# Performance work log

Measured on AMD Instinct MI355X. Metric: run time of the kernel, lower is better.

Reference implementation:

```python
import jax, jax.numpy as jnp
import numpy as np

B, T, C, H = 2, 2048, 1024, 16
D = C // H  # head dim = 64

def setup_inputs() -> dict:
    key = jax.random.key(0)
    k1, k2, k3 = jax.random.split(key, 3)
    x = jax.random.normal(k1, (B, T, C), dtype=jnp.float32)
    Wqkv = jax.random.normal(k2, (C, 3 * C), dtype=jnp.float32) * (1.0 / np.sqrt(C))
    bqkv = jnp.zeros((3 * C,), dtype=jnp.float32)
    Wo = jax.random.normal(k3, (C, C), dtype=jnp.float32) * (1.0 / np.sqrt(C))
    bo = jnp.zeros((C,), dtype=jnp.float32)
    return {"x": x, "Wqkv": Wqkv, "bqkv": bqkv, "Wo": Wo, "bo": bo}

def reference(x, Wqkv, bqkv, Wo, bo):
    b, t, c = x.shape
    qkv = x @ Wqkv + bqkv                              # [B,T,3C]
    q, k, v = jnp.split(qkv, 3, axis=-1)
    # [B,T,C] -> [B,H,T,D]
    q = q.reshape(b, t, H, D).transpose(0, 2, 1, 3)
    k = k.reshape(b, t, H, D).transpose(0, 2, 1, 3)
    v = v.reshape(b, t, H, D).transpose(0, 2, 1, 3)
    scores = jnp.einsum('bhqd,bhkd->bhqk', q, k) * (1.0 / np.sqrt(D))
    causal = jnp.tril(jnp.ones((t, t), dtype=bool))
    scores = jnp.where(causal, scores, -jnp.inf)
    probs = jax.nn.softmax(scores, axis=-1)           # dropout p=0 -> identity
    out = jnp.einsum('bhqk,bhkd->bhqd', probs, v)
    out = out.transpose(0, 2, 1, 3).reshape(b, t, c)
    return out @ Wo + bo
```

## Files before the change

### kernel.cpp

```cpp
#include <hip/hip_runtime.h>
#include <hip/hip_bf16.h>

typedef __attribute__((ext_vector_type(8))) short bf16x8;
typedef __attribute__((ext_vector_type(4))) short bf16x4;
typedef __attribute__((ext_vector_type(4))) float f32x4;

static __device__ __forceinline__ __hip_bfloat16 f2b(float f) {
    return __float2bfloat16(f);
}
static __device__ __forceinline__ unsigned pack2(float a, float b) {
    unsigned ua = (unsigned)__bfloat16_as_ushort(__float2bfloat16(a));
    unsigned ub = (unsigned)__bfloat16_as_ushort(__float2bfloat16(b));
    return ua | (ub << 16);
}
static __device__ __forceinline__ float exp2fast(float x) {
    return __builtin_amdgcn_exp2f(x);
}

#define QSCALE 0.1803368801111f

__global__ __launch_bounds__(256) void k_prep(
    const float* __restrict__ x, __hip_bfloat16* __restrict__ xb,
    const float* __restrict__ Wqkv, __hip_bfloat16* __restrict__ WqkvT,
    const float* __restrict__ Wo, __hip_bfloat16* __restrict__ WoT)
{
    const int bx = blockIdx.x;
    if (bx < 2048) {
        int i = bx * 256 + threadIdx.x;
        const int stride = 2048 * 256;
        for (; i < 1048576; i += stride) {
            float4 v = reinterpret_cast<const float4*>(x)[i];
            __hip_bfloat16* o = xb + 4 * (size_t)i;
            o[0] = f2b(v.x); o[1] = f2b(v.y); o[2] = f2b(v.z); o[3] = f2b(v.w);
        }
        return;
    }
    __shared__ float tile[32][33];
    const float* in;
    __hip_bfloat16* outp;
    int R, Cn, c0, r0;
    if (bx < 5120) {
        const int b = bx - 2048;
        in = Wqkv; outp = WqkvT; R = 1024; Cn = 3072;
        c0 = (b % 96) * 32; r0 = (b / 96) * 32;
    } else {
        const int b = bx - 5120;
        in = Wo; outp = WoT; R = 1024; Cn = 1024;
        c0 = (b & 31) * 32; r0 = (b >> 5) * 32;
    }
    const int tx = threadIdx.x & 31, ty = threadIdx.x >> 5;
#pragma unroll
    for (int i = 0; i < 32; i += 8)
        tile[ty + i][tx] = in[(size_t)(r0 + ty + i) * Cn + c0 + tx];
    __syncthreads();
#pragma unroll
    for (int i = 0; i < 32; i += 8)
        outp[(size_t)(c0 + ty + i) * R + r0 + tx] = f2b(tile[tx][ty + i]);
}

#define QK_STAGE(buf, kt)                                                       \
    {                                                                           \
        const int k0_ = (kt) << 5;                                              \
        _Pragma("unroll")                                                       \
        for (int i = 0; i < 2; ++i) {                                           \
            const int idx = i * 256 + tid;                                      \
            const int r_ = idx >> 2;                                            \
            const int j_ = idx & 3;                                             \
            const int js_ = j_ ^ ((r_ >> 1) & 3);                               \
            __builtin_amdgcn_global_load_lds(                                   \
                (const __attribute__((address_space(1))) void*)(A + (size_t)(m0 + r_) * K + k0_ + js_ * 8), \
                (__attribute__((address_space(3))) void*)(&As[buf][r_][j_ * 8]), 16, 0, 0); \
        }                                                                       \
        _Pragma("unroll")                                                       \
        for (int i = 0; i < 2; ++i) {                                           \
            const int idx = i * 256 + tid;                                      \
            const int r_ = idx >> 2;                                            \
            const int j_ = idx & 3;                                             \
            const int js_ = j_ ^ ((r_ >> 1) & 3);                               \
            __builtin_amdgcn_global_load_lds(                                   \
                (const __attribute__((address_space(1))) void*)(Bt + (size_t)(n0 + r_) * K + k0_ + js_ * 8), \
                (__attribute__((address_space(3))) void*)(&Bs[buf][r_][j_ * 8]), 16, 0, 0); \
        }                                                                       \
    }

__global__ __launch_bounds__(256, 3) void k_gemm_qkv(
    const __hip_bfloat16* __restrict__ A,
    const __hip_bfloat16* __restrict__ Bt,
    const float* __restrict__ bias,
    int K,
    __hip_bfloat16* __restrict__ Qb,
    __hip_bfloat16* __restrict__ Kb,
    __hip_bfloat16* __restrict__ Vt)
{
    __shared__ __hip_bfloat16 As[3][128][32];
    __shared__ __hip_bfloat16 Bs[3][128][32];

    const int tid = threadIdx.x;
    const int lane = tid & 63;
    const int wid = tid >> 6;
    const int wm = wid >> 1, wn = wid & 1;
    const int m0 = blockIdx.y * 128, n0 = blockIdx.x * 128;
    const int l15 = lane & 15, lg = lane >> 4;
    const int rchunk = (lg ^ ((l15 >> 1) & 3)) * 8;

    f32x4 acc[4][4] = {};
    const int nt = K >> 5;

    QK_STAGE(0, 0);
    QK_STAGE(1, 1);
    asm volatile("s_waitcnt vmcnt(4)" ::: "memory");
    __builtin_amdgcn_sched_barrier(0);
    __builtin_amdgcn_s_barrier();
    __builtin_amdgcn_sched_barrier(0);

    for (int t = 0; t < nt; ++t) {
        const int cur = t % 3;
        if (t + 2 < nt) {
            const int nxt = (t + 2) % 3;
            QK_STAGE(nxt, t + 2);
        }
        bf16x8 a[4], bb[4];
#pragma unroll
        for (int m = 0; m < 4; ++m)
            a[m] = *(const bf16x8*)&As[cur][wm * 64 + m * 16 + l15][rchunk];
#pragma unroll
        for (int n = 0; n < 4; ++n)
            bb[n] = *(const bf16x8*)&Bs[cur][wn * 64 + n * 16 + l15][rchunk];
        __builtin_amdgcn_s_setprio(1);
#pragma unroll
        for (int m = 0; m < 4; ++m)
#pragma unroll
            for (int n = 0; n < 4; ++n)
                acc[m][n] = __builtin_amdgcn_mfma_f32_16x16x32_bf16(a[m], bb[n], acc[m][n], 0, 0, 0);
        __builtin_amdgcn_s_setprio(0);
        __builtin_amdgcn_sched_barrier(0);
        if (t + 2 < nt)
            asm volatile("s_waitcnt vmcnt(4)" ::: "memory");
        else
            asm volatile("s_waitcnt vmcnt(0)" ::: "memory");
        __builtin_amdgcn_sched_barrier(0);
        __builtin_amdgcn_s_barrier();
        __builtin_amdgcn_sched_barrier(0);
    }

#pragma unroll
    for (int m = 0; m < 4; ++m) {
        const int row = m0 + wm * 64 + m * 16 + lg * 4;
#pragma unroll
        for (int n = 0; n < 4; ++n) {
            const int col = n0 + wn * 64 + n * 16 + l15;
            const float bv = bias[col];
#pragma unroll
            for (int r = 0; r < 4; ++r) {
                const float val = acc[m][n][r] + bv;
                const int rr = row + r;
                const int sec = col >> 10, cw = col & 1023;
                const int hh = cw >> 6, d = cw & 63;
                const int bq = rr >> 11, tt = rr & 2047;
                const int bh = bq * 16 + hh;
                if (sec == 0)
                    Qb[((size_t)bh * 2048 + tt) * 64 + d] = f2b(val * QSCALE);
                else if (sec == 1)
                    Kb[((size_t)bh * 2048 + tt) * 64 + d] = f2b(val);
                else
                    Vt[((size_t)bh * 64 + d) * 2048 + tt] = f2b(val);
            }
        }
    }
}

#define OUT_STAGE(buf, kt)                                                      \
    {                                                                           \
        const int k0_ = (kt) << 5;                                              \
        _Pragma("unroll")                                                       \
        for (int i = 0; i < 2; ++i) {                                           \
            const int idx = i * 256 + tid;                                      \
            const int r_ = idx >> 2;                                            \
            const int j_ = idx & 3;                                             \
            const int js_ = j_ ^ ((r_ >> 1) & 3);                               \
            __builtin_amdgcn_global_load_lds(                                   \
                (const __attribute__((address_space(1))) void*)(A + (size_t)(m0 + r_) * K + k0_ + js_ * 8), \
                (__attribute__((address_space(3))) void*)(&As[buf][r_][j_ * 8]), 16, 0, 0); \
        }                                                                       \
        {                                                                       \
            const int r_ = tid >> 2;                                            \
            const int j_ = tid & 3;                                             \
            const int js_ = j_ ^ ((r_ >> 1) & 3);                               \
            __builtin_amdgcn_global_load_lds(                                   \
                (const __attribute__((address_space(1))) void*)(Bt + (size_t)(n0 + r_) * K + k0_ + js_ * 8), \
                (__attribute__((address_space(3))) void*)(&Bs[buf][r_][j_ * 8]), 16, 0, 0); \
        }                                                                       \
    }

__global__ __launch_bounds__(256, 4) void k_gemm_out(
    const __hip_bfloat16* __restrict__ A,
    const __hip_bfloat16* __restrict__ Bt,
    const float* __restrict__ bias,
    int K, int Nn,
    float* __restrict__ outf)
{
    __shared__ __hip_bfloat16 As[3][128][32];
    __shared__ __hip_bfloat16 Bs[3][64][32];

    const int tid = threadIdx.x;
    const int lane = tid & 63;
    const int wid = tid >> 6;
    const int wm = wid >> 1, wn = wid & 1;
    const int m0 = blockIdx.y * 128, n0 = blockIdx.x * 64;
    const int l15 = lane & 15, lg = lane >> 4;
    const int rchunk = (lg ^ ((l15 >> 1) & 3)) * 8;

    f32x4 acc[4][2] = {};
    const int nt = K >> 5;

    OUT_STAGE(0, 0);
    OUT_STAGE(1, 1);
    asm volatile("s_waitcnt vmcnt(3)" ::: "memory");
    __builtin_amdgcn_sched_barrier(0);
    __builtin_amdgcn_s_barrier();
    __builtin_amdgcn_sched_barrier(0);

    for (int t = 0; t < nt; ++t) {
        const int cur = t % 3;
        if (t + 2 < nt) {
            const int nxt = (t + 2) % 3;
            OUT_STAGE(nxt, t + 2);
        }
        bf16x8 a[4], bb[2];
#pragma unroll
        for (int m = 0; m < 4; ++m)
            a[m] = *(const bf16x8*)&As[cur][wm * 64 + m * 16 + l15][rchunk];
#pragma unroll
        for (int n = 0; n < 2; ++n)
            bb[n] = *(const bf16x8*)&Bs[cur][wn * 32 + n * 16 + l15][rchunk];
        __builtin_amdgcn_s_setprio(1);
#pragma unroll
        for (int m = 0; m < 4; ++m)
#pragma unroll
            for (int n = 0; n < 2; ++n)
                acc[m][n] = __builtin_amdgcn_mfma_f32_16x16x32_bf16(a[m], bb[n], acc[m][n], 0, 0, 0);
        __builtin_amdgcn_s_setprio(0);
        __builtin_amdgcn_sched_barrier(0);
        if (t + 2 < nt)
            asm volatile("s_waitcnt vmcnt(3)" ::: "memory");
        else
            asm volatile("s_waitcnt vmcnt(0)" ::: "memory");
        __builtin_amdgcn_sched_barrier(0);
        __builtin_amdgcn_s_barrier();
        __builtin_amdgcn_sched_barrier(0);
    }

#pragma unroll
    for (int m = 0; m < 4; ++m) {
        const int row = m0 + wm * 64 + m * 16 + lg * 4;
#pragma unroll
        for (int n = 0; n < 2; ++n) {
            const int col = n0 + wn * 32 + n * 16 + l15;
            const float bv = bias[col];
#pragma unroll
            for (int r = 0; r < 4; ++r)
                outf[(size_t)(row + r) * Nn + col] = acc[m][n][r] + bv;
        }
    }
}

#define DEFER_THR 4.0f

#define AT_STAGE(buf, tt)                                                       \
    {                                                                           \
        const int ks_ = (tt) << 6;                                              \
        _Pragma("unroll")                                                       \
        for (int i = 0; i < 4; ++i) {                                           \
            const int idx = i * 128 + tid;                                      \
            const int r_ = idx >> 3;                                            \
            const int j_ = idx & 7;                                             \
            const int js_ = j_ ^ (r_ & 7);                                      \
            __builtin_amdgcn_global_load_lds(                                   \
                (const __attribute__((address_space(1))) void*)(Kbase + (size_t)(ks_ + r_) * 64 + js_ * 8), \
                (__attribute__((address_space(3))) void*)(&Ks[buf][r_][j_ * 8]), 16, 0, 0); \
        }                                                                       \
        _Pragma("unroll")                                                       \
        for (int i = 0; i < 4; ++i) {                                           \
            const int idx = i * 128 + tid;                                      \
            const int r_ = idx >> 3;                                            \
            const int j_ = idx & 7;                                             \
            const int js_ = j_ ^ (r_ & 7);                                      \
            __builtin_amdgcn_global_load_lds(                                   \
                (const __attribute__((address_space(1))) void*)(Vbase + (size_t)r_ * 2048 + ks_ + js_ * 8), \
                (__attribute__((address_space(3))) void*)(&Vs[buf][r_][j_ * 8]), 16, 0, 0); \
        }                                                                       \
    }

#define FULL_STEP_L(BUF)                                                        \
    {                                                                           \
        bf16x8 bk0[4], bk1[4];                                                  \
        _Pragma("unroll")                                                       \
        for (int kf = 0; kf < 4; ++kf) {                                        \
            bk0[kf] = *(const bf16x8*)&Ks[BUF][kf * 16 + l15][(lg ^ kswz) * 8]; \
            bk1[kf] = *(const bf16x8*)&Ks[BUF][kf * 16 + l15][((4 + lg) ^ kswz) * 8]; \
        }                                                                       \
        f32x4 s0[4] = {}, s1[4] = {};                                           \
        __builtin_amdgcn_s_setprio(1);                                          \
        _Pragma("unroll")                                                       \
        for (int kf = 0; kf < 4; ++kf) {                                        \
            s0[kf] = __builtin_amdgcn_mfma_f32_16x16x32_bf16(bk0[kf], aq[0][0], s0[kf], 0, 0, 0); \
            s0[kf] = __builtin_amdgcn_mfma_f32_16x16x32_bf16(bk1[kf], aq[0][1], s0[kf], 0, 0, 0); \
            s1[kf] = __builtin_amdgcn_mfma_f32_16x16x32_bf16(bk0[kf], aq[1][0], s1[kf], 0, 0, 0); \
            s1[kf] = __builtin_amdgcn_mfma_f32_16x16x32_bf16(bk1[kf], aq[1][1], s1[kf], 0, 0, 0); \
        }                                                                       \
        __builtin_amdgcn_s_setprio(0);                                          \
        float px0 = fmaxf(fmaxf(fmaxf(s0[0][0], s0[0][1]), fmaxf(s0[0][2], s0[0][3])), \
                          fmaxf(fmaxf(s0[1][0], s0[1][1]), fmaxf(s0[1][2], s0[1][3]))); \
        px0 = fmaxf(px0, fmaxf(fmaxf(fmaxf(s0[2][0], s0[2][1]), fmaxf(s0[2][2], s0[2][3])), \
                               fmaxf(fmaxf(s0[3][0], s0[3][1]), fmaxf(s0[3][2], s0[3][3])))); \
        float px1 = fmaxf(fmaxf(fmaxf(s1[0][0], s1[0][1]), fmaxf(s1[0][2], s1[0][3])), \
                          fmaxf(fmaxf(s1[1][0], s1[1][1]), fmaxf(s1[1][2], s1[1][3]))); \
        px1 = fmaxf(px1, fmaxf(fmaxf(fmaxf(s1[2][0], s1[2][1]), fmaxf(s1[2][2], s1[2][3])), \
                               fmaxf(fmaxf(s1[3][0], s1[3][1]), fmaxf(s1[3][2], s1[3][3])))); \
        px0 = fmaxf(px0, __shfl_xor(px0, 16));                                  \
        px0 = fmaxf(px0, __shfl_xor(px0, 32));                                  \
        px1 = fmaxf(px1, __shfl_xor(px1, 16));                                  \
        px1 = fmaxf(px1, __shfl_xor(px1, 32));                                  \
        if (__any((px0 > m0 + DEFER_THR) || (px1 > m1 + DEFER_THR))) {          \
            const float mn0 = fmaxf(m0, px0), mn1 = fmaxf(m1, px1);             \
            const float al0 = exp2fast(m0 - mn0), al1 = exp2fast(m1 - mn1);     \
            m0 = mn0; m1 = mn1;                                                 \
            l0 *= al0; l1 *= al1;                                               \
            _Pragma("unroll")                                                   \
            for (int dc = 0; dc < 4; ++dc)                                      \
                _Pragma("unroll")                                               \
                for (int r = 0; r < 4; ++r) {                                   \
                    o[0][dc][r] *= al0;                                         \
                    o[1][dc][r] *= al1;                                         \
                }                                                               \
        }                                                                       \
        float rs0 = 0.f, rs1 = 0.f;                                             \
        _Pragma("unroll")                                                       \
        for (int kf = 0; kf < 4; ++kf) {                                        \
            _Pragma("unroll")                                                   \
            for (int r = 0; r < 4; ++r) {                                       \
                s0[kf][r] = exp2fast(s0[kf][r] - m0);                           \
                s1[kf][r] = exp2fast(s1[kf][r] - m1);                           \
                rs0 += s0[kf][r];                                               \
                rs1 += s1[kf][r];                                               \
            }                                                                   \
            uint2 w0, w1;                                                       \
            w0.x = pack2(s0[kf][0], s0[kf][1]); w0.y = pack2(s0[kf][2], s0[kf][3]); \
            w1.x = pack2(s1[kf][0], s1[kf][1]); w1.y = pack2(s1[kf][2], s1[kf][3]); \
            const int off = l15 * 64 + ((kf * 16 + lg * 4) ^ swz);              \
            *(uint2*)&Pw0[off] = w0;                                            \
            *(uint2*)&Pw1[off] = w1;                                            \
        }                                                                       \
        rs0 += __shfl_xor(rs0, 16); rs0 += __shfl_xor(rs0, 32);                 \
        rs1 += __shfl_xor(rs1, 16); rs1 += __shfl_xor(rs1, 32);                 \
        l0 += rs0; l1 += rs1;                                                   \
        _Pragma("unroll")                                                       \
        for (int c2 = 0; c2 < 2; ++c2) {                                        \
            bf16x8 bv[4];                                                       \
            _Pragma("unroll")                                                   \
            for (int dc = 0; dc < 4; ++dc)                                      \
                bv[dc] = *(const bf16x8*)&Vs[BUF][dc * 16 + l15][(((c2 << 2) | lg) ^ kswz) * 8]; \
            const int off = l15 * 64 + ((c2 * 32 + lg * 8) ^ swz);              \
            const bf16x8 pb0 = *(const bf16x8*)&Pw0[off];                       \
            const bf16x8 pb1 = *(const bf16x8*)&Pw1[off];                       \
            __builtin_amdgcn_s_setprio(1);                                      \
            _Pragma("unroll")                                                   \
            for (int dc = 0; dc < 4; ++dc) {                                    \
                o[0][dc] = __builtin_amdgcn_mfma_f32_16x16x32_bf16(bv[dc], pb0, o[0][dc], 0, 0, 0); \
                o[1][dc] = __builtin_amdgcn_mfma_f32_16x16x32_bf16(bv[dc], pb1, o[1][dc], 0, 0, 0); \
            }                                                                   \
            __builtin_amdgcn_s_setprio(0);                                      \
        }                                                                       \
    }

#define TAIL_STEP_L(BUF)                                                        \
    {                                                                           \
        const int ks_ = nfull * 64;                                             \
        float mr[2] = {m0, m1}, lr[2] = {l0, l1};                               \
        _Pragma("unroll")                                                       \
        for (int qf = 0; qf < 2; ++qf) {                                        \
            const int qlo = qw + qf * 16;                                       \
            const int qv = qlo + l15;                                           \
            bf16x8 bk0[4], bk1[4];                                              \
            _Pragma("unroll")                                                   \
            for (int kf = 0; kf < 4; ++kf) {                                    \
                bk0[kf] = *(const bf16x8*)&Ks[BUF][kf * 16 + l15][(lg ^ kswz) * 8]; \
                bk1[kf] = *(const bf16x8*)&Ks[BUF][kf * 16 + l15][((4 + lg) ^ kswz) * 8]; \
            }                                                                   \
            f32x4 s[4] = {};                                                    \
            _Pragma("unroll")                                                   \
            for (int kf = 0; kf < 4; ++kf) {                                    \
                if (ks_ + kf * 16 <= qlo + 15) {                                \
                    s[kf] = __builtin_amdgcn_mfma_f32_16x16x32_bf16(bk0[kf], aq[qf][0], s[kf], 0, 0, 0); \
                    s[kf] = __builtin_amdgcn_mfma_f32_16x16x32_bf16(bk1[kf], aq[qf][1], s[kf], 0, 0, 0); \
                }                                                               \
            }                                                                   \
            const int kb = ks_ + lg * 4;                                        \
            _Pragma("unroll")                                                   \
            for (int kf = 0; kf < 4; ++kf)                                      \
                _Pragma("unroll")                                               \
                for (int r = 0; r < 4; ++r)                                     \
                    s[kf][r] = (kb + kf * 16 + r <= qv) ? s[kf][r] : -1e30f;    \
            float mx = fmaxf(fmaxf(fmaxf(s[0][0], s[0][1]), fmaxf(s[0][2], s[0][3])), \
                             fmaxf(fmaxf(s[1][0], s[1][1]), fmaxf(s[1][2], s[1][3]))); \
            mx = fmaxf(mx, fmaxf(fmaxf(fmaxf(s[2][0], s[2][1]), fmaxf(s[2][2], s[2][3])), \
                                 fmaxf(fmaxf(s[3][0], s[3][1]), fmaxf(s[3][2], s[3][3])))); \
            mx = fmaxf(mx, __shfl_xor(mx, 16));                                 \
            mx = fmaxf(mx, __shfl_xor(mx, 32));                                 \
            const float mnew = fmaxf(mr[qf], mx);                               \
            const float al = exp2fast(mr[qf] - mnew);                           \
            mr[qf] = mnew;                                                      \
            float rs = 0.f;                                                     \
            _Pragma("unroll")                                                   \
            for (int kf = 0; kf < 4; ++kf)                                      \
                _Pragma("unroll")                                               \
                for (int r = 0; r < 4; ++r) {                                   \
                    s[kf][r] = exp2fast(s[kf][r] - mnew);                       \
                    rs += s[kf][r];                                             \
                }                                                               \
            rs += __shfl_xor(rs, 16);                                           \
            rs += __shfl_xor(rs, 32);                                           \
            lr[qf] = lr[qf] * al + rs;                                          \
            _Pragma("unroll")                                                   \
            for (int dc = 0; dc < 4; ++dc)                                      \
                _Pragma("unroll")                                               \
                for (int r = 0; r < 4; ++r) o[qf][dc][r] *= al;                 \
            __hip_bfloat16* Pw = (qf == 0) ? Pw0 : Pw1;                         \
            _Pragma("unroll")                                                   \
            for (int kf = 0; kf < 4; ++kf) {                                    \
                uint2 w;                                                        \
                w.x = pack2(s[kf][0], s[kf][1]);                                \
                w.y = pack2(s[kf][2], s[kf][3]);                                \
                *(uint2*)&Pw[l15 * 64 + ((kf * 16 + lg * 4) ^ swz)] = w;        \
            }                                                                   \
            _Pragma("unroll")                                                   \
            for (int c2 = 0; c2 < 2; ++c2) {                                    \
                if (ks_ + c2 * 32 <= qlo + 15) {                                \
                    bf16x8 bv[4];                                               \
                    _Pragma("unroll")                                           \
                    for (int dc = 0; dc < 4; ++dc)                              \
                        bv[dc] = *(const bf16x8*)&Vs[BUF][dc * 16 + l15][(((c2 << 2) | lg) ^ kswz) * 8]; \
                    const bf16x8 pb = *(const bf16x8*)&Pw[l15 * 64 + ((c2 * 32 + lg * 8) ^ swz)]; \
                    _Pragma("unroll")                                           \
                    for (int dc = 0; dc < 4; ++dc)                              \
                        o[qf][dc] = __builtin_amdgcn_mfma_f32_16x16x32_bf16(bv[dc], pb, o[qf][dc], 0, 0, 0); \
                }                                                               \
            }                                                                   \
        }                                                                       \
        l0 = lr[0]; l1 = lr[1];                                                 \
    }

__global__ __launch_bounds__(128, 2) void k_attn(
    const __hip_bfloat16* __restrict__ Qb,
    const __hip_bfloat16* __restrict__ Kb,
    const __hip_bfloat16* __restrict__ Vt,
    __hip_bfloat16* __restrict__ att)
{
    __shared__ __hip_bfloat16 Ks[2][64][64];
    __shared__ __hip_bfloat16 Vs[2][64][64];
    __shared__ __hip_bfloat16 P_lds[2][2][16 * 64];
    const int tid = threadIdx.x, lane = tid & 63, wid = tid >> 6;
    const int lid = blockIdx.x;
    const int xcd = lid & 7, j = lid >> 3;
    const int bh = xcd * 4 + (j & 3);
    const int v = j >> 2;
    const int tile = (v < 8) ? (31 - v) : ((v < 16) ? (v - 8) : ((v < 24) ? (39 - v) : (v - 16)));
    const int q0 = tile * 64;
    const int qw = q0 + wid * 32;
    const int l15 = lane & 15, lg = lane >> 4;
    const int swz = (l15 & 7) << 3;
    const int kswz = l15 & 7;

    const __hip_bfloat16* Qbase = Qb + (size_t)bh * 2048 * 64;
    const __hip_bfloat16* Kbase = Kb + (size_t)bh * 2048 * 64;
    const __hip_bfloat16* Vbase = Vt + (size_t)bh * 64 * 2048;

    bf16x8 aq[2][2];
#pragma unroll
    for (int qf = 0; qf < 2; ++qf)
#pragma unroll
        for (int c = 0; c < 2; ++c)
            aq[qf][c] = *(const bf16x8*)(Qbase + (size_t)(qw + qf * 16 + l15) * 64 + c * 32 + lg * 8);

    f32x4 o[2][4] = {};
    float m0 = -1e30f, m1 = -1e30f, l0 = 0.f, l1 = 0.f;

    const int nfull = qw >> 6;
    const int NT = tile + 1;
    __hip_bfloat16* Pw0 = &P_lds[wid][0][0];
    __hip_bfloat16* Pw1 = &P_lds[wid][1][0];

    AT_STAGE(0, 0);
    __syncthreads();

    int cur = 0;
    for (int tt = 0; tt < NT; ++tt) {
        if (tt + 1 < NT) AT_STAGE(cur ^ 1, tt + 1);
        if (tt < nfull) {
            FULL_STEP_L(cur);
        } else {
            TAIL_STEP_L(cur);
        }
        __syncthreads();
        cur ^= 1;
    }

    const int bq = bh >> 4, hh = bh & 15;
    const float inv0 = 1.0f / l0, inv1 = 1.0f / l1;
#pragma unroll
    for (int qf = 0; qf < 2; ++qf) {
        const float inv = (qf == 0) ? inv0 : inv1;
        const size_t rowb = ((size_t)(bq * 2048 + qw + qf * 16 + l15)) * 1024 + hh * 64;
#pragma unroll
        for (int dc = 0; dc < 4; ++dc) {
            bf16x4 st;
#pragma unroll
            for (int r = 0; r < 4; ++r)
                st[r] = (short)__bfloat16_as_ushort(__float2bfloat16(o[qf][dc][r] * inv));
            *(bf16x4*)(att + rowb + dc * 16 + lg * 4) = st;
        }
    }
}

extern "C" void kernel_launch(void* const* d_in, const int* in_sizes, int n_in,
                              void* d_out, int out_size, void* d_ws, size_t ws_size,
                              hipStream_t stream)
{
    const float* x    = (const float*)d_in[0];
    const float* Wqkv = (const float*)d_in[1];
    const float* bqkv = (const float*)d_in[2];
    const float* Wo   = (const float*)d_in[3];
    const float* bo   = (const float*)d_in[4];
    float* out = (float*)d_out;

    char* ws = (char*)d_ws;
    const size_t MB = 1024 * 1024;
    __hip_bfloat16* xb    = (__hip_bfloat16*)(ws);
    __hip_bfloat16* WqkvT = (__hip_bfloat16*)(ws + 8 * MB);
    __hip_bfloat16* WoT   = (__hip_bfloat16*)(ws + 14 * MB);
    __hip_bfloat16* Qb    = (__hip_bfloat16*)(ws + 16 * MB);
    __hip_bfloat16* Kb    = (__hip_bfloat16*)(ws + 24 * MB);
    __hip_bfloat16* Vt    = (__hip_bfloat16*)(ws + 32 * MB);
    __hip_bfloat16* att   = (__hip_bfloat16*)(ws + 40 * MB);

    k_prep<<<6144, 256, 0, stream>>>(x, xb, Wqkv, WqkvT, Wo, WoT);

    k_gemm_qkv<<<dim3(24, 32), 256, 0, stream>>>(
        xb, WqkvT, bqkv, 1024, Qb, Kb, Vt);

    k_attn<<<1024, 128, 0, stream>>>(Qb, Kb, Vt, att);

    k_gemm_out<<<dim3(16, 32), 256, 0, stream>>>(
        att, WoT, bo, 1024, 1024, out);
}
```

Before: 127.7 us.

## Split attention query tile across four waves of sixteen rows each

The attention kernel moves from 2 waves handling 32 query rows each to 4 waves handling 16 rows each, so the block grows to 256 threads with launch bounds of 4 blocks per CU. The cooperative K/V staging loop is halved to match the larger thread count, and each wave keeps one set of softmax state and accumulators. This lowers per-wave register pressure and raises the number of resident waves to hide latency. In exchange, each K/V fragment read from LDS now feeds half as many MFMAs, so LDS read traffic per FLOP doubles.

```diff
diff --git a/kernel.cpp b/kernel.cpp
--- a/kernel.cpp
+++ b/kernel.cpp
@@ -270,8 +270,8 @@
     {                                                                           \
         const int ks_ = (tt) << 6;                                              \
         _Pragma("unroll")                                                       \
-        for (int i = 0; i < 4; ++i) {                                           \
-            const int idx = i * 128 + tid;                                      \
+        for (int i = 0; i < 2; ++i) {                                           \
+            const int idx = i * 256 + tid;                                      \
             const int r_ = idx >> 3;                                            \
             const int j_ = idx & 7;                                             \
             const int js_ = j_ ^ (r_ & 7);                                      \
@@ -280,8 +280,8 @@
                 (__attribute__((address_space(3))) void*)(&Ks[buf][r_][j_ * 8]), 16, 0, 0); \
         }                                                                       \
         _Pragma("unroll")                                                       \
-        for (int i = 0; i < 4; ++i) {                                           \
-            const int idx = i * 128 + tid;                                      \
+        for (int i = 0; i < 2; ++i) {                                           \
+            const int idx = i * 256 + tid;                                      \
             const int r_ = idx >> 3;                                            \
             const int j_ = idx & 7;                                             \
             const int js_ = j_ ^ (r_ & 7);                                      \
@@ -299,76 +299,56 @@
             bk0[kf] = *(const bf16x8*)&Ks[BUF][kf * 16 + l15][(lg ^ kswz) * 8]; \
             bk1[kf] = *(const bf16x8*)&Ks[BUF][kf * 16 + l15][((4 + lg) ^ kswz) * 8]; \
         }                                                                       \
-        f32x4 s0[4] = {}, s1[4] = {};                                           \
+        f32x4 s[4] = {};                                                        \
         __builtin_amdgcn_s_setprio(1);                                          \
         _Pragma("unroll")                                                       \
         for (int kf = 0; kf < 4; ++kf) {                                        \
-            s0[kf] = __builtin_amdgcn_mfma_f32_16x16x32_bf16(bk0[kf], aq[0][0], s0[kf], 0, 0, 0); \
-            s0[kf] = __builtin_amdgcn_mfma_f32_16x16x32_bf16(bk1[kf], aq[0][1], s0[kf], 0, 0, 0); \
-            s1[kf] = __builtin_amdgcn_mfma_f32_16x16x32_bf16(bk0[kf], aq[1][0], s1[kf], 0, 0, 0); \
-            s1[kf] = __builtin_amdgcn_mfma_f32_16x16x32_bf16(bk1[kf], aq[1][1], s1[kf], 0, 0, 0); \
+            s[kf] = __builtin_amdgcn_mfma_f32_16x16x32_bf16(bk0[kf], aq0, s[kf], 0, 0, 0); \
+            s[kf] = __builtin_amdgcn_mfma_f32_16x16x32_bf16(bk1[kf], aq1, s[kf], 0, 0, 0); \
         }                                                                       \
         __builtin_amdgcn_s_setprio(0);                                          \
-        float px0 = fmaxf(fmaxf(fmaxf(s0[0][0], s0[0][1]), fmaxf(s0[0][2], s0[0][3])), \
-                          fmaxf(fmaxf(s0[1][0], s0[1][1]), fmaxf(s0[1][2], s0[1][3]))); \
-        px0 = fmaxf(px0, fmaxf(fmaxf(fmaxf(s0[2][0], s0[2][1]), fmaxf(s0[2][2], s0[2][3])), \
-                               fmaxf(fmaxf(s0[3][0], s0[3][1]), fmaxf(s0[3][2], s0[3][3])))); \
-        float px1 = fmaxf(fmaxf(fmaxf(s1[0][0], s1[0][1]), fmaxf(s1[0][2], s1[0][3])), \
-                          fmaxf(fmaxf(s1[1][0], s1[1][1]), fmaxf(s1[1][2], s1[1][3]))); \
-        px1 = fmaxf(px1, fmaxf(fmaxf(fmaxf(s1[2][0], s1[2][1]), fmaxf(s1[2][2], s1[2][3])), \
-                               fmaxf(fmaxf(s1[3][0], s1[3][1]), fmaxf(s1[3][2], s1[3][3])))); \
-        px0 = fmaxf(px0, __shfl_xor(px0, 16));                                  \
-        px0 = fmaxf(px0, __shfl_xor(px0, 32));                                  \
-        px1 = fmaxf(px1, __shfl_xor(px1, 16));                                  \
-        px1 = fmaxf(px1, __shfl_xor(px1, 32));                                  \
-        if (__any((px0 > m0 + DEFER_THR) || (px1 > m1 + DEFER_THR))) {          \
-            const float mn0 = fmaxf(m0, px0), mn1 = fmaxf(m1, px1);             \
-            const float al0 = exp2fast(m0 - mn0), al1 = exp2fast(m1 - mn1);     \
-            m0 = mn0; m1 = mn1;                                                 \
-            l0 *= al0; l1 *= al1;                                               \
+        float px = fmaxf(fmaxf(fmaxf(s[0][0], s[0][1]), fmaxf(s[0][2], s[0][3])), \
+                         fmaxf(fmaxf(s[1][0], s[1][1]), fmaxf(s[1][2], s[1][3]))); \
+        px = fmaxf(px, fmaxf(fmaxf(fmaxf(s[2][0], s[2][1]), fmaxf(s[2][2], s[2][3])), \
+                             fmaxf(fmaxf(s[3][0], s[3][1]), fmaxf(s[3][2], s[3][3])))); \
+        px = fmaxf(px, __shfl_xor(px, 16));                                     \
+        px = fmaxf(px, __shfl_xor(px, 32));                                     \
+        if (__any(px > m0 + DEFER_THR)) {                                       \
+            const float mn_ = fmaxf(m0, px);                                    \
+            const float al_ = exp2fast(m0 - mn_);                               \
+            m0 = mn_; l0 *= al_;                                                \
             _Pragma("unroll")                                                   \
             for (int dc = 0; dc < 4; ++dc)                                      \
                 _Pragma("unroll")                                               \
-                for (int r = 0; r < 4; ++r) {                                   \
-                    o[0][dc][r] *= al0;                                         \
-                    o[1][dc][r] *= al1;                                         \
-                }                                                               \
-        }                                                                       \
-        float rs0 = 0.f, rs1 = 0.f;                                             \
+                for (int r = 0; r < 4; ++r) o[dc][r] *= al_;                    \
+        }                                                                       \
+        float rs_ = 0.f;                                                        \
         _Pragma("unroll")                                                       \
         for (int kf = 0; kf < 4; ++kf) {                                        \
             _Pragma("unroll")                                                   \
             for (int r = 0; r < 4; ++r) {                                       \
-                s0[kf][r] = exp2fast(s0[kf][r] - m0);                           \
-                s1[kf][r] = exp2fast(s1[kf][r] - m1);                           \
-                rs0 += s0[kf][r];                                               \
-                rs1 += s1[kf][r];                                               \
+                s[kf][r] = exp2fast(s[kf][r] - m0);                             \
+                rs_ += s[kf][r];                                                \
             }                                                                   \
-            uint2 w0, w1;                                                       \
-            w0.x = pack2(s0[kf][0], s0[kf][1]); w0.y = pack2(s0[kf][2], s0[kf][3]); \
-            w1.x = pack2(s1[kf][0], s1[kf][1]); w1.y = pack2(s1[kf][2], s1[kf][3]); \
-            const int off = l15 * 64 + ((kf * 16 + lg * 4) ^ swz);              \
-            *(uint2*)&Pw0[off] = w0;                                            \
-            *(uint2*)&Pw1[off] = w1;                                            \
-        }                                                                       \
-        rs0 += __shfl_xor(rs0, 16); rs0 += __shfl_xor(rs0, 32);                 \
-        rs1 += __shfl_xor(rs1, 16); rs1 += __shfl_xor(rs1, 32);                 \
-        l0 += rs0; l1 += rs1;                                                   \
+            uint2 w_;                                                           \
+            w_.x = pack2(s[kf][0], s[kf][1]);                                   \
+            w_.y = pack2(s[kf][2], s[kf][3]);                                   \
+            *(uint2*)&Pw[l15 * 64 + ((kf * 16 + lg * 4) ^ swz)] = w_;           \
+        }                                                                       \
+        rs_ += __shfl_xor(rs_, 16);                                             \
+        rs_ += __shfl_xor(rs_, 32);                                             \
+        l0 += rs_;                                                              \
         _Pragma("unroll")                                                       \
         for (int c2 = 0; c2 < 2; ++c2) {                                        \
             bf16x8 bv[4];                                                       \
             _Pragma("unroll")                                                   \
             for (int dc = 0; dc < 4; ++dc)                                      \
                 bv[dc] = *(const bf16x8*)&Vs[BUF][dc * 16 + l15][(((c2 << 2) | lg) ^ kswz) * 8]; \
-            const int off = l15 * 64 + ((c2 * 32 + lg * 8) ^ swz);              \
-            const bf16x8 pb0 = *(const bf16x8*)&Pw0[off];                       \
-            const bf16x8 pb1 = *(const bf16x8*)&Pw1[off];                       \
+            const bf16x8 pb = *(const bf16x8*)&Pw[l15 * 64 + ((c2 * 32 + lg * 8) ^ swz)]; \
             __builtin_amdgcn_s_setprio(1);                                      \
             _Pragma("unroll")                                                   \
-            for (int dc = 0; dc < 4; ++dc) {                                    \
-                o[0][dc] = __builtin_amdgcn_mfma_f32_16x16x32_bf16(bv[dc], pb0, o[0][dc], 0, 0, 0); \
-                o[1][dc] = __builtin_amdgcn_mfma_f32_16x16x32_bf16(bv[dc], pb1, o[1][dc], 0, 0, 0); \
-            }                                                                   \
+            for (int dc = 0; dc < 4; ++dc)                                      \
+                o[dc] = __builtin_amdgcn_mfma_f32_16x16x32_bf16(bv[dc], pb, o[dc], 0, 0, 0); \
             __builtin_amdgcn_s_setprio(0);                                      \
         }                                                                       \
     }
@@ -376,81 +356,74 @@
 #define TAIL_STEP_L(BUF)                                                        \
     {                                                                           \
         const int ks_ = nfull * 64;                                             \
-        float mr[2] = {m0, m1}, lr[2] = {l0, l1};                               \
-        _Pragma("unroll")                                                       \
-        for (int qf = 0; qf < 2; ++qf) {                                        \
-            const int qlo = qw + qf * 16;                                       \
-            const int qv = qlo + l15;                                           \
-            bf16x8 bk0[4], bk1[4];                                              \
-            _Pragma("unroll")                                                   \
-            for (int kf = 0; kf < 4; ++kf) {                                    \
-                bk0[kf] = *(const bf16x8*)&Ks[BUF][kf * 16 + l15][(lg ^ kswz) * 8]; \
-                bk1[kf] = *(const bf16x8*)&Ks[BUF][kf * 16 + l15][((4 + lg) ^ kswz) * 8]; \
+        const int qv = qw + l15;                                                \
+        bf16x8 bk0[4], bk1[4];                                                  \
+        _Pragma("unroll")                                                       \
+        for (int kf = 0; kf < 4; ++kf) {                                        \
+            bk0[kf] = *(const bf16x8*)&Ks[BUF][kf * 16 + l15][(lg ^ kswz) * 8]; \
+            bk1[kf] = *(const bf16x8*)&Ks[BUF][kf * 16 + l15][((4 + lg) ^ kswz) * 8]; \
+        }                                                                       \
+        f32x4 s[4] = {};                                                        \
+        _Pragma("unroll")                                                       \
+        for (int kf = 0; kf < 4; ++kf) {                                        \
+            if (ks_ + kf * 16 <= qw + 15) {                                     \
+                s[kf] = __builtin_amdgcn_mfma_f32_16x16x32_bf16(bk0[kf], aq0, s[kf], 0, 0, 0); \
+                s[kf] = __builtin_amdgcn_mfma_f32_16x16x32_bf16(bk1[kf], aq1, s[kf], 0, 0, 0); \
             }                                                                   \
-            f32x4 s[4] = {};                                                    \
-            _Pragma("unroll")                                                   \
-            for (int kf = 0; kf < 4; ++kf) {                                    \
-                if (ks_ + kf * 16 <= qlo + 15) {                                \
-                    s[kf] = __builtin_amdgcn_mfma_f32_16x16x32_bf16(bk0[kf], aq[qf][0], s[kf], 0, 0, 0); \
-                    s[kf] = __builtin_amdgcn_mfma_f32_16x16x32_bf16(bk1[kf], aq[qf][1], s[kf], 0, 0, 0); \
-                }                                                               \
+        }                                                                       \
+        const int kb = ks_ + lg * 4;                                            \
+        _Pragma("unroll")                                                       \
+        for (int kf = 0; kf < 4; ++kf)                                          \
+            _Pragma("unroll")                                                   \
+            for (int r = 0; r < 4; ++r)                                         \
+                s[kf][r] = (kb + kf * 16 + r <= qv) ? s[kf][r] : -1e30f;        \
+        float mx = fmaxf(fmaxf(fmaxf(s[0][0], s[0][1]), fmaxf(s[0][2], s[0][3])), \
+                         fmaxf(fmaxf(s[1][0], s[1][1]), fmaxf(s[1][2], s[1][3]))); \
+        mx = fmaxf(mx, fmaxf(fmaxf(fmaxf(s[2][0], s[2][1]), fmaxf(s[2][2], s[2][3])), \
+                             fmaxf(fmaxf(s[3][0], s[3][1]), fmaxf(s[3][2], s[3][3])))); \
+        mx = fmaxf(mx, __shfl_xor(mx, 16));                                     \
+        mx = fmaxf(mx, __shfl_xor(mx, 32));                                     \
+        const float mnew = fmaxf(m0, mx);                                       \
+        const float al_ = exp2fast(m0 - mnew);                                  \
+        m0 = mnew;                                                              \
+        float rs_ = 0.f;                                                        \
+        _Pragma("unroll")                                                       \
+        for (int kf = 0; kf < 4; ++kf)                                          \
+            _Pragma("unroll")                                                   \
+            for (int r = 0; r < 4; ++r) {                                       \
+                s[kf][r] = exp2fast(s[kf][r] - mnew);                           \
+                rs_ += s[kf][r];                                                \
             }                                                                   \
-            const int kb = ks_ + lg * 4;                                        \
-            _Pragma("unroll")                                                   \
-            for (int kf = 0; kf < 4; ++kf)                                      \
+        rs_ += __shfl_xor(rs_, 16);                                             \
+        rs_ += __shfl_xor(rs_, 32);                                             \
+        l0 = l0 * al_ + rs_;                                                    \
+        _Pragma("unroll")                                                       \
+        for (int dc = 0; dc < 4; ++dc)                                          \
+            _Pragma("unroll")                                                   \
+            for (int r = 0; r < 4; ++r) o[dc][r] *= al_;                        \
+        _Pragma("unroll")                                                       \
+        for (int kf = 0; kf < 4; ++kf) {                                        \
+            uint2 w_;                                                           \
+            w_.x = pack2(s[kf][0], s[kf][1]);                                   \
+            w_.y = pack2(s[kf][2], s[kf][3]);                                   \
+            *(uint2*)&Pw[l15 * 64 + ((kf * 16 + lg * 4) ^ swz)] = w_;           \
+        }                                                                       \
+        _Pragma("unroll")                                                       \
+        for (int c2 = 0; c2 < 2; ++c2) {                                        \
+            if (ks_ + c2 * 32 <= qw + 15) {                                     \
+                bf16x8 bv[4];                                                   \
                 _Pragma("unroll")                                               \
-                for (int r = 0; r < 4; ++r)                                     \
-                    s[kf][r] = (kb + kf * 16 + r <= qv) ? s[kf][r] : -1e30f;    \
-            float mx = fmaxf(fmaxf(fmaxf(s[0][0], s[0][1]), fmaxf(s[0][2], s[0][3])), \
-                             fmaxf(fmaxf(s[1][0], s[1][1]), fmaxf(s[1][2], s[1][3]))); \
-            mx = fmaxf(mx, fmaxf(fmaxf(fmaxf(s[2][0], s[2][1]), fmaxf(s[2][2], s[2][3])), \
-                                 fmaxf(fmaxf(s[3][0], s[3][1]), fmaxf(s[3][2], s[3][3])))); \
-            mx = fmaxf(mx, __shfl_xor(mx, 16));                                 \
-            mx = fmaxf(mx, __shfl_xor(mx, 32));                                 \
-            const float mnew = fmaxf(mr[qf], mx);                               \
-            const float al = exp2fast(mr[qf] - mnew);                           \
-            mr[qf] = mnew;                                                      \
-            float rs = 0.f;                                                     \
-            _Pragma("unroll")                                                   \
-            for (int kf = 0; kf < 4; ++kf)                                      \
+                for (int dc = 0; dc < 4; ++dc)                                  \
+                    bv[dc] = *(const bf16x8*)&Vs[BUF][dc * 16 + l15][(((c2 << 2) | lg) ^ kswz) * 8]; \
+                const bf16x8 pb = *(const bf16x8*)&Pw[l15 * 64 + ((c2 * 32 + lg * 8) ^ swz)]; \
                 _Pragma("unroll")                                               \
-                for (int r = 0; r < 4; ++r) {                                   \
-                    s[kf][r] = exp2fast(s[kf][r] - mnew);                       \
-                    rs += s[kf][r];                                             \
-                }                                                               \
-            rs += __shfl_xor(rs, 16);                                           \
-            rs += __shfl_xor(rs, 32);                                           \
-            lr[qf] = lr[qf] * al + rs;                                          \
-            _Pragma("unroll")                                                   \
-            for (int dc = 0; dc < 4; ++dc)                                      \
-                _Pragma("unroll")                                               \
-                for (int r = 0; r < 4; ++r) o[qf][dc][r] *= al;                 \
-            __hip_bfloat16* Pw = (qf == 0) ? Pw0 : Pw1;                         \
-            _Pragma("unroll")                                                   \
-            for (int kf = 0; kf < 4; ++kf) {                                    \
-                uint2 w;                                                        \
-                w.x = pack2(s[kf][0], s[kf][1]);                                \
-                w.y = pack2(s[kf][2], s[kf][3]);                                \
-                *(uint2*)&Pw[l15 * 64 + ((kf * 16 + lg * 4) ^ swz)] = w;        \
+                for (int dc = 0; dc < 4; ++dc)                                  \
+                    o[dc] = __builtin_amdgcn_mfma_f32_16x16x32_bf16(bv[dc], pb, o[dc], 0, 0, 0); \
             }                                                                   \
-            _Pragma("unroll")                                                   \
-            for (int c2 = 0; c2 < 2; ++c2) {                                    \
-                if (ks_ + c2 * 32 <= qlo + 15) {                                \
-                    bf16x8 bv[4];                                               \
-                    _Pragma("unroll")                                           \
-                    for (int dc = 0; dc < 4; ++dc)                              \
-                        bv[dc] = *(const bf16x8*)&Vs[BUF][dc * 16 + l15][(((c2 << 2) | lg) ^ kswz) * 8]; \
-                    const bf16x8 pb = *(const bf16x8*)&Pw[l15 * 64 + ((c2 * 32 + lg * 8) ^ swz)]; \
-                    _Pragma("unroll")                                           \
-                    for (int dc = 0; dc < 4; ++dc)                              \
-                        o[qf][dc] = __builtin_amdgcn_mfma_f32_16x16x32_bf16(bv[dc], pb, o[qf][dc], 0, 0, 0); \
-                }                                                               \
-            }                                                                   \
-        }                                                                       \
-        l0 = lr[0]; l1 = lr[1];                                                 \
-    }
-
-__global__ __launch_bounds__(128, 2) void k_attn(
+        }                                                                       \
+    }
+
+__global__ __launch_bounds__(256, 4) void k_attn(
     const __hip_bfloat16* __restrict__ Qb,
     const __hip_bfloat16* __restrict__ Kb,
     const __hip_bfloat16* __restrict__ Vt,
@@ -458,7 +431,7 @@
 {
     __shared__ __hip_bfloat16 Ks[2][64][64];
     __shared__ __hip_bfloat16 Vs[2][64][64];
-    __shared__ __hip_bfloat16 P_lds[2][2][16 * 64];
+    __shared__ __hip_bfloat16 P_lds[4][16 * 64];
     const int tid = threadIdx.x, lane = tid & 63, wid = tid >> 6;
     const int lid = blockIdx.x;
     const int xcd = lid & 7, j = lid >> 3;
@@ -466,7 +439,7 @@
     const int v = j >> 2;
     const int tile = (v < 8) ? (31 - v) : ((v < 16) ? (v - 8) : ((v < 24) ? (39 - v) : (v - 16)));
     const int q0 = tile * 64;
-    const int qw = q0 + wid * 32;
+    const int qw = q0 + wid * 16;
     const int l15 = lane & 15, lg = lane >> 4;
     const int swz = (l15 & 7) << 3;
     const int kswz = l15 & 7;
@@ -475,20 +448,15 @@
     const __hip_bfloat16* Kbase = Kb + (size_t)bh * 2048 * 64;
     const __hip_bfloat16* Vbase = Vt + (size_t)bh * 64 * 2048;
 
-    bf16x8 aq[2][2];
-#pragma unroll
-    for (int qf = 0; qf < 2; ++qf)
-#pragma unroll
-        for (int c = 0; c < 2; ++c)
-            aq[qf][c] = *(const bf16x8*)(Qbase + (size_t)(qw + qf * 16 + l15) * 64 + c * 32 + lg * 8);
-
-    f32x4 o[2][4] = {};
-    float m0 = -1e30f, m1 = -1e30f, l0 = 0.f, l1 = 0.f;
+    const bf16x8 aq0 = *(const bf16x8*)(Qbase + (size_t)(qw + l15) * 64 + lg * 8);
+    const bf16x8 aq1 = *(const bf16x8*)(Qbase + (size_t)(qw + l15) * 64 + 32 + lg * 8);
+
+    f32x4 o[4] = {};
+    float m0 = -1e30f, l0 = 0.f;
 
     const int nfull = qw >> 6;
     const int NT = tile + 1;
-    __hip_bfloat16* Pw0 = &P_lds[wid][0][0];
-    __hip_bfloat16* Pw1 = &P_lds[wid][1][0];
+    __hip_bfloat16* Pw = &P_lds[wid][0];
 
     AT_STAGE(0, 0);
     __syncthreads();
@@ -506,19 +474,15 @@
     }
 
     const int bq = bh >> 4, hh = bh & 15;
-    const float inv0 = 1.0f / l0, inv1 = 1.0f / l1;
-#pragma unroll
-    for (int qf = 0; qf < 2; ++qf) {
-        const float inv = (qf == 0) ? inv0 : inv1;
-        const size_t rowb = ((size_t)(bq * 2048 + qw + qf * 16 + l15)) * 1024 + hh * 64;
-#pragma unroll
-        for (int dc = 0; dc < 4; ++dc) {
-            bf16x4 st;
-#pragma unroll
-            for (int r = 0; r < 4; ++r)
-                st[r] = (short)__bfloat16_as_ushort(__float2bfloat16(o[qf][dc][r] * inv));
-            *(bf16x4*)(att + rowb + dc * 16 + lg * 4) = st;
-        }
+    const float inv = 1.0f / l0;
+    const size_t rowb = ((size_t)(bq * 2048 + qw + l15)) * 1024 + hh * 64;
+#pragma unroll
+    for (int dc = 0; dc < 4; ++dc) {
+        bf16x4 st;
+#pragma unroll
+        for (int r = 0; r < 4; ++r)
+            st[r] = (short)__bfloat16_as_ushort(__float2bfloat16(o[dc][r] * inv));
+        *(bf16x4*)(att + rowb + dc * 16 + lg * 4) = st;
     }
 }
 
@@ -548,7 +512,7 @@
     k_gemm_qkv<<<dim3(24, 32), 256, 0, stream>>>(
         xb, WqkvT, bqkv, 1024, Qb, Kb, Vt);
 
-    k_attn<<<1024, 128, 0, stream>>>(Qb, Kb, Vt, att);
+    k_attn<<<1024, 256, 0, stream>>>(Qb, Kb, Vt, att);
 
     k_gemm_out<<<dim3(16, 32), 256, 0, stream>>>(
         att, WoT, bo, 1024, 1024, out);
```

Measured after the change: 116.1 us. 1.1x faster.
